# Kernel tuning notes

Hardware: AMD Instinct MI355X
Metric: run time of the kernel (lower is better)

Reference implementation:

```python
import jax, jax.numpy as jnp
import numpy as np

D = 1024
H = 16
DH = D // H  # 64
SCALE = DH ** (-0.5)

def setup_inputs() -> dict:
    key = jax.random.key(0)
    k1, k2, k3, k4, k5 = jax.random.split(key, 5)
    x = jax.random.normal(k1, (4, 2048, D), dtype=jnp.float32)
    w_qkv = jax.random.normal(k2, (D, 3 * D), dtype=jnp.float32) * (D ** -0.5)
    b_qkv = jax.random.normal(k3, (3 * D,), dtype=jnp.float32) * 0.02
    w_out = jax.random.normal(k4, (D, D), dtype=jnp.float32) * (D ** -0.5)
    b_out = jax.random.normal(k5, (D,), dtype=jnp.float32) * 0.02
    return {"x": x, "w_qkv": w_qkv, "b_qkv": b_qkv, "w_out": w_out, "b_out": b_out}

def reference(x, w_qkv, b_qkv, w_out, b_out):
    B, S, C = x.shape
    qkv = x @ w_qkv + b_qkv                          # [B,S,3D]
    qkv = qkv.reshape(B, S, 3, H, DH)
    qkv = jnp.transpose(qkv, (0, 3, 2, 1, 4))        # [B,H,3,S,DH]
    q, k, v = qkv[:, :, 0], qkv[:, :, 1], qkv[:, :, 2]
    q = q * SCALE
    scores = jnp.einsum('bhqd,bhkd->bhqk', q, k)     # [B,H,S,S]
    attn = jax.nn.softmax(scores.astype(jnp.float32), axis=-1).astype(scores.dtype)
    out = jnp.einsum('bhqk,bhkd->bhqd', attn, v)     # [B,H,S,DH]
    out = jnp.transpose(out, (0, 2, 1, 3)).reshape(B, S, C)
    return out @ w_out + b_out
```

## Files before the change

kernel.cpp:

```cpp
#include <hip/hip_runtime.h>

#define D_ 1024
#define H_ 16
#define DH_ 64
#define S_ 2048
#define B_ 4
#define N_ (B_*S_)
#define M3_ 3072
#define QSC_ 0.18033688011112042f

typedef _Float16 f16;
typedef _Float16 f16x8 __attribute__((ext_vector_type(8)));
typedef _Float16 f16x4 __attribute__((ext_vector_type(4)));
typedef _Float16 f16x2 __attribute__((ext_vector_type(2)));
typedef __fp16   h16x2 __attribute__((ext_vector_type(2)));
typedef float    f32x4 __attribute__((ext_vector_type(4)));

typedef __attribute__((address_space(1))) void gvoid;
typedef __attribute__((address_space(3))) void lvoid;

__device__ __forceinline__ void gl16(const f16* g, f16* l) {
    __builtin_amdgcn_global_load_lds((gvoid*)g, (lvoid*)l, 16, 0, 0);
}

__device__ __forceinline__ f16x2 pk_cvt(float a, float b) {
#if __has_builtin(__builtin_amdgcn_cvt_pkrtz)
    h16x2 t = __builtin_amdgcn_cvt_pkrtz(a, b);
    return __builtin_bit_cast(f16x2, t);
#else
    f16x2 r; r[0] = (f16)a; r[1] = (f16)b; return r;
#endif
}

__device__ __forceinline__ float dot2acc(f16x2 a, float acc) {
#if __has_builtin(__builtin_amdgcn_fdot2)
    h16x2 one; one[0] = (__fp16)1.f; one[1] = (__fp16)1.f;
    return __builtin_amdgcn_fdot2(__builtin_bit_cast(h16x2, a), one, acc, false);
#else
    return acc + (float)a[0] + (float)a[1];
#endif
}

__global__ __launch_bounds__(256) void cvt_x_kernel(const float* __restrict__ in,
                                                    f16* __restrict__ out) {
    size_t i = ((size_t)blockIdx.x * 256 + threadIdx.x) * 4;
    float4 f = *reinterpret_cast<const float4*>(in + i);
    f16x4 o;
    o[0] = (f16)f.x; o[1] = (f16)f.y; o[2] = (f16)f.z; o[3] = (f16)f.w;
    *reinterpret_cast<f16x4*>(out + i) = o;
}

__global__ __launch_bounds__(256) void wt_cvt_kernel(const float* __restrict__ in,
                                                     f16* __restrict__ out,
                                                     int K, int Nc) {
    __shared__ float tile[32][33];
    int tx = threadIdx.x & 31, ty = threadIdx.x >> 5;
    int c = blockIdx.x * 32 + tx;
    #pragma unroll
    for (int i = 0; i < 4; i++) {
        int r = blockIdx.y * 32 + ty + i * 8;
        tile[ty + i * 8][tx] = in[(size_t)r * Nc + c];
    }
    __syncthreads();
    #pragma unroll
    for (int i = 0; i < 4; i++) {
        int r2 = blockIdx.x * 32 + ty + i * 8;
        int c2 = blockIdx.y * 32 + tx;
        out[(size_t)r2 * K + c2] = (f16)tile[tx][ty + i * 8];
    }
}

__global__ __launch_bounds__(256) void gemm_qkv_kernel(
        const f16* __restrict__ A, const f16* __restrict__ Bt,
        const float* __restrict__ bias,
        f16* __restrict__ qo, f16* __restrict__ ko, f16* __restrict__ vTo) {
    __shared__ __align__(16) f16 As[128 * 32];
    __shared__ __align__(16) f16 Bs[128 * 32];
    const int tid  = threadIdx.x;
    const int lane = tid & 63, w = tid >> 6;
    const int quad = lane >> 4, lrow = lane & 15;
    const int wm = (w & 1) * 64, wn = (w >> 1) * 64;
    const int n0 = blockIdx.x * 128, m0 = blockIdx.y * 128;

    f32x4 acc[4][4];
    #pragma unroll
    for (int i = 0; i < 4; i++)
        #pragma unroll
        for (int j = 0; j < 4; j++) acc[i][j] = {0.f, 0.f, 0.f, 0.f};

    const int ar0 = tid >> 2, ap0 = tid & 3;
    const f16* Ag0 = A  + (size_t)(n0 + ar0) * D_ + ap0 * 8;
    const f16* Ag1 = Ag0 + (size_t)64 * D_;
    const f16* Bg0 = Bt + (size_t)(m0 + ar0) * D_ + ap0 * 8;
    const f16* Bg1 = Bg0 + (size_t)64 * D_;
    f16* Asl = As + tid * 8;
    f16* Bsl = Bs + tid * 8;

    for (int kt = 0; kt < D_ / 32; kt++) {
        gl16(Ag0 + kt * 32, Asl);
        gl16(Ag1 + kt * 32, Asl + 64 * 32);
        gl16(Bg0 + kt * 32, Bsl);
        gl16(Bg1 + kt * 32, Bsl + 64 * 32);
        __syncthreads();
        f16x8 af[4], bf[4];
        #pragma unroll
        for (int i = 0; i < 4; i++)
            af[i] = *reinterpret_cast<const f16x8*>(&As[(wm + i * 16 + lrow) * 32 + quad * 8]);
        #pragma unroll
        for (int j = 0; j < 4; j++)
            bf[j] = *reinterpret_cast<const f16x8*>(&Bs[(wn + j * 16 + lrow) * 32 + quad * 8]);
        #pragma unroll
        for (int i = 0; i < 4; i++)
            #pragma unroll
            for (int j = 0; j < 4; j++)
                acc[i][j] = __builtin_amdgcn_mfma_f32_16x16x32_f16(af[i], bf[j], acc[i][j], 0, 0, 0);
        __syncthreads();
    }

    #pragma unroll
    for (int j = 0; j < 4; j++) {
        int m   = m0 + wn + j * 16 + lrow;
        int sec = m >> 10;
        int hd  = m & 1023;
        int hh  = hd >> 6, d = hd & 63;
        float bb = bias[m];
        if (sec == 2) {
            #pragma unroll
            for (int i = 0; i < 4; i++) {
                int n = n0 + wm + i * 16 + quad * 4;
                int bidx = n >> 11, s = n & 2047;
                f16x4 o;
                #pragma unroll
                for (int r = 0; r < 4; r++) o[r] = (f16)(acc[i][j][r] + bb);
                *reinterpret_cast<f16x4*>(
                    &vTo[(((size_t)(bidx * H_ + hh)) * DH_ + d) * S_ + s]) = o;
            }
        } else {
            f16* dst = (sec == 0) ? qo : ko;
            float sc = (sec == 0) ? QSC_ : 1.0f;
            #pragma unroll
            for (int i = 0; i < 4; i++) {
                #pragma unroll
                for (int r = 0; r < 4; r++) {
                    int n = n0 + wm + i * 16 + quad * 4 + r;
                    int bidx = n >> 11, s = n & 2047;
                    dst[(((size_t)(bidx * H_ + hh)) * S_ + s) * DH_ + d] =
                        (f16)((acc[i][j][r] + bb) * sc);
                }
            }
        }
    }
}

__global__ __launch_bounds__(256) void attn_kernel(
        const f16* __restrict__ q, const f16* __restrict__ k,
        const f16* __restrict__ vT, f16* __restrict__ ctx) {
    __shared__ __align__(16) f16 Ks[128 * 72];
    __shared__ __align__(16) f16 Vs[64 * 136];
    const int tid  = threadIdx.x;
    const int lane = tid & 63, w = tid >> 6;
    const int quad = lane >> 4, lrow = lane & 15;
    const int bh = blockIdx.y;
    const int b  = bh >> 4, h = bh & 15;
    const int q0 = blockIdx.x * 256;
    const f16* qb = q  + (size_t)bh * S_ * DH_;
    const f16* kb = k  + (size_t)bh * S_ * DH_;
    const f16* vb = vT + (size_t)bh * DH_ * S_;

    f16x8 qf[4][2];
    #pragma unroll
    for (int f = 0; f < 4; f++)
        #pragma unroll
        for (int hf = 0; hf < 2; hf++)
            qf[f][hf] = *reinterpret_cast<const f16x8*>(
                qb + (size_t)(q0 + w * 64 + f * 16 + lrow) * DH_ + hf * 32 + quad * 8);

    float l_i[4] = {0.f, 0.f, 0.f, 0.f};
    f32x4 ot[4][4];
    #pragma unroll
    for (int f = 0; f < 4; f++)
        #pragma unroll
        for (int dj = 0; dj < 4; dj++) ot[f][dj] = {0.f, 0.f, 0.f, 0.f};

    int kslot[4], kpart[4], vrow[4], vpart[4];
    #pragma unroll
    for (int i = 0; i < 4; i++) {
        int ch = tid + i * 256;
        int g = ch >> 3, jj = g & 7, qd = (g >> 3) & 3;
        kslot[i] = (g & ~31) + ((jj >> 2) << 4) + (qd << 2) + (jj & 3);
        kpart[i] = ch & 7;
        vrow[i] = ch >> 4; vpart[i] = ch & 15;
    }

    f16x8 krg[4], vrg[4];
    #pragma unroll
    for (int i = 0; i < 4; i++) {
        int ch = tid + i * 256;
        krg[i] = *reinterpret_cast<const f16x8*>(kb + (size_t)(ch >> 3) * DH_ + (ch & 7) * 8);
        vrg[i] = *reinterpret_cast<const f16x8*>(vb + (size_t)vrow[i] * S_ + vpart[i] * 8);
    }

    for (int kt = 0; kt < S_ / 128; kt++) {
        #pragma unroll
        for (int i = 0; i < 4; i++) {
            *reinterpret_cast<f16x8*>(&Ks[kslot[i] * 72 + kpart[i] * 8]) = krg[i];
            *reinterpret_cast<f16x8*>(&Vs[vrow[i] * 136 + vpart[i] * 8]) = vrg[i];
        }
        __syncthreads();
        if (kt + 1 < S_ / 128) {
            const int kv1 = (kt + 1) * 128;
            #pragma unroll
            for (int i = 0; i < 4; i++) {
                int ch = tid + i * 256;
                krg[i] = *reinterpret_cast<const f16x8*>(kb + (size_t)(kv1 + (ch >> 3)) * DH_ + (ch & 7) * 8);
                vrg[i] = *reinterpret_cast<const f16x8*>(vb + (size_t)vrow[i] * S_ + kv1 + vpart[i] * 8);
            }
        }

        #pragma unroll
        for (int t = 0; t < 4; t++) {
            f16x8 p8[4];
            #pragma unroll
            for (int half = 0; half < 2; half++) {
                int mb = 2 * t + half;
                f16x8 kf0 = *reinterpret_cast<const f16x8*>(&Ks[(mb * 16 + lrow) * 72 + quad * 8]);
                f16x8 kf1 = *reinterpret_cast<const f16x8*>(&Ks[(mb * 16 + lrow) * 72 + 32 + quad * 8]);
                #pragma unroll
                for (int f = 0; f < 4; f++) {
                    f32x4 st = {0.f, 0.f, 0.f, 0.f};
                    st = __builtin_amdgcn_mfma_f32_16x16x32_f16(kf0, qf[f][0], st, 0, 0, 0);
                    st = __builtin_amdgcn_mfma_f32_16x16x32_f16(kf1, qf[f][1], st, 0, 0, 0);
                    f16x2 lo = pk_cvt(__builtin_amdgcn_exp2f(st[0]),
                                      __builtin_amdgcn_exp2f(st[1]));
                    f16x2 hi = pk_cvt(__builtin_amdgcn_exp2f(st[2]),
                                      __builtin_amdgcn_exp2f(st[3]));
                    l_i[f] = dot2acc(lo, l_i[f]);
                    l_i[f] = dot2acc(hi, l_i[f]);
                    p8[f][half * 4 + 0] = lo[0]; p8[f][half * 4 + 1] = lo[1];
                    p8[f][half * 4 + 2] = hi[0]; p8[f][half * 4 + 3] = hi[1];
                }
            }
            #pragma unroll
            for (int dj = 0; dj < 4; dj++) {
                f16x8 vf = *reinterpret_cast<const f16x8*>(
                    &Vs[(dj * 16 + lrow) * 136 + t * 32 + quad * 8]);
                #pragma unroll
                for (int f = 0; f < 4; f++)
                    ot[f][dj] = __builtin_amdgcn_mfma_f32_16x16x32_f16(vf, p8[f], ot[f][dj], 0, 0, 0);
            }
        }
        __syncthreads();
    }

    #pragma unroll
    for (int f = 0; f < 4; f++) {
        float l = l_i[f];
        l += __shfl_xor(l, 16);
        l += __shfl_xor(l, 32);
        float inv = 1.0f / l;
        int qrow = q0 + w * 64 + f * 16 + lrow;
        #pragma unroll
        for (int dj = 0; dj < 4; dj++) {
            f16x4 o;
            #pragma unroll
            for (int r = 0; r < 4; r++) o[r] = (f16)(ot[f][dj][r] * inv);
            *reinterpret_cast<f16x4*>(
                &ctx[((size_t)(b * S_ + qrow)) * D_ + h * DH_ + dj * 16 + quad * 4]) = o;
        }
    }
}

__global__ __launch_bounds__(256) void gemm_out_kernel(
        const f16* __restrict__ A, const f16* __restrict__ Bt,
        const float* __restrict__ bias, float* __restrict__ out) {
    __shared__ __align__(16) f16 As[128 * 32];
    __shared__ __align__(16) f16 Bs[128 * 32];
    const int tid  = threadIdx.x;
    const int lane = tid & 63, w = tid >> 6;
    const int quad = lane >> 4, lrow = lane & 15;
    const int wm = (w & 1) * 64, wn = (w >> 1) * 64;
    const int n0 = blockIdx.x * 128, m0 = blockIdx.y * 128;

    f32x4 acc[4][4];
    #pragma unroll
    for (int i = 0; i < 4; i++)
        #pragma unroll
        for (int j = 0; j < 4; j++) acc[i][j] = {0.f, 0.f, 0.f, 0.f};

    const int ar0 = tid >> 2, ap0 = tid & 3;
    const f16* Ag0 = A  + (size_t)(n0 + ar0) * D_ + ap0 * 8;
    const f16* Ag1 = Ag0 + (size_t)64 * D_;
    const f16* Bg0 = Bt + (size_t)(m0 + ar0) * D_ + ap0 * 8;
    const f16* Bg1 = Bg0 + (size_t)64 * D_;
    f16* Asl = As + tid * 8;
    f16* Bsl = Bs + tid * 8;

    for (int kt = 0; kt < D_ / 32; kt++) {
        gl16(Ag0 + kt * 32, Asl);
        gl16(Ag1 + kt * 32, Asl + 64 * 32);
        gl16(Bg0 + kt * 32, Bsl);
        gl16(Bg1 + kt * 32, Bsl + 64 * 32);
        __syncthreads();
        f16x8 af[4], bf[4];
        #pragma unroll
        for (int i = 0; i < 4; i++)
            af[i] = *reinterpret_cast<const f16x8*>(&As[(wm + i * 16 + lrow) * 32 + quad * 8]);
        #pragma unroll
        for (int j = 0; j < 4; j++)
            bf[j] = *reinterpret_cast<const f16x8*>(&Bs[(wn + j * 16 + lrow) * 32 + quad * 8]);
        #pragma unroll
        for (int i = 0; i < 4; i++)
            #pragma unroll
            for (int j = 0; j < 4; j++)
                acc[i][j] = __builtin_amdgcn_mfma_f32_16x16x32_f16(af[i], bf[j], acc[i][j], 0, 0, 0);
        __syncthreads();
    }

    #pragma unroll
    for (int j = 0; j < 4; j++) {
        int m = m0 + wn + j * 16 + lrow;
        float bb = bias[m];
        #pragma unroll
        for (int i = 0; i < 4; i++)
            #pragma unroll
            for (int r = 0; r < 4; r++) {
                int n = n0 + wm + i * 16 + quad * 4 + r;
                out[(size_t)n * D_ + m] = acc[i][j][r] + bb;
            }
    }
}

extern "C" void kernel_launch(void* const* d_in, const int* in_sizes, int n_in,
                              void* d_out, int out_size, void* d_ws, size_t ws_size,
                              hipStream_t stream) {
    (void)in_sizes; (void)n_in; (void)out_size; (void)ws_size;
    const float* x     = (const float*)d_in[0];
    const float* w_qkv = (const float*)d_in[1];
    const float* b_qkv = (const float*)d_in[2];
    const float* w_out = (const float*)d_in[3];
    const float* b_out = (const float*)d_in[4];
    float* out = (float*)d_out;

    char* ws = (char*)d_ws;
    const size_t MB = 1024 * 1024;
    f16* xb    = (f16*)(ws);
    f16* wqkvT = (f16*)(ws + 16 * MB);
    f16* woutT = (f16*)(ws + 22 * MB);
    f16* qs    = (f16*)(ws + 24 * MB);
    f16* kk    = (f16*)(ws + 40 * MB);
    f16* vTb   = (f16*)(ws + 72 * MB);
    f16* ctx   = xb;

    cvt_x_kernel<<<(N_ * D_) / (256 * 4), 256, 0, stream>>>(x, xb);
    wt_cvt_kernel<<<dim3(M3_ / 32, D_ / 32), 256, 0, stream>>>(w_qkv, wqkvT, D_, M3_);
    wt_cvt_kernel<<<dim3(D_ / 32, D_ / 32), 256, 0, stream>>>(w_out, woutT, D_, D_);
    gemm_qkv_kernel<<<dim3(N_ / 128, M3_ / 128), 256, 0, stream>>>(xb, wqkvT, b_qkv, qs, kk, vTb);
    attn_kernel<<<dim3(S_ / 256, B_ * H_), 256, 0, stream>>>(qs, kk, vTb, ctx);
    gemm_out_kernel<<<dim3(N_ / 128, D_ / 128), 256, 0, stream>>>(ctx, woutT, b_out, out);
}
```

Measured before the change: 274.9 us.

## Load attention K/V fragments directly from global memory, drop LDS staging

The attention kernel no longer stages K and V tiles through shared memory with barriers. Each lane now loads its MFMA fragments straight from global memory, relying on L2/L1 caching because the four waves read the same K/V data. The 1-D grid is remapped so blocks on the same head are spread across XCDs to improve L2 locality. This removes the LDS writes and syncthreads, but adds redundant global/cache traffic and exposes memory latency, since there is no software prefetch.

```diff
diff --git a/kernel.cpp b/kernel.cpp
--- a/kernel.cpp
+++ b/kernel.cpp
@@ -155,14 +155,13 @@
 __global__ __launch_bounds__(256) void attn_kernel(
         const f16* __restrict__ q, const f16* __restrict__ k,
         const f16* __restrict__ vT, f16* __restrict__ ctx) {
-    __shared__ __align__(16) f16 Ks[128 * 72];
-    __shared__ __align__(16) f16 Vs[64 * 136];
     const int tid  = threadIdx.x;
     const int lane = tid & 63, w = tid >> 6;
     const int quad = lane >> 4, lrow = lane & 15;
-    const int bh = blockIdx.y;
+    const int id = blockIdx.x;
+    const int bh = (id & 7) * 8 + (id >> 6);
     const int b  = bh >> 4, h = bh & 15;
-    const int q0 = blockIdx.x * 256;
+    const int q0 = ((id >> 3) & 7) * 256;
     const f16* qb = q  + (size_t)bh * S_ * DH_;
     const f16* kb = k  + (size_t)bh * S_ * DH_;
     const f16* vb = vT + (size_t)bh * DH_ * S_;
@@ -182,49 +181,23 @@
         #pragma unroll
         for (int dj = 0; dj < 4; dj++) ot[f][dj] = {0.f, 0.f, 0.f, 0.f};
 
-    int kslot[4], kpart[4], vrow[4], vpart[4];
-    #pragma unroll
-    for (int i = 0; i < 4; i++) {
-        int ch = tid + i * 256;
-        int g = ch >> 3, jj = g & 7, qd = (g >> 3) & 3;
-        kslot[i] = (g & ~31) + ((jj >> 2) << 4) + (qd << 2) + (jj & 3);
-        kpart[i] = ch & 7;
-        vrow[i] = ch >> 4; vpart[i] = ch & 15;
-    }
-
-    f16x8 krg[4], vrg[4];
-    #pragma unroll
-    for (int i = 0; i < 4; i++) {
-        int ch = tid + i * 256;
-        krg[i] = *reinterpret_cast<const f16x8*>(kb + (size_t)(ch >> 3) * DH_ + (ch & 7) * 8);
-        vrg[i] = *reinterpret_cast<const f16x8*>(vb + (size_t)vrow[i] * S_ + vpart[i] * 8);
-    }
+    const int krow_lane = ((lrow >> 2) << 3) + (lrow & 3);
+    const f16* kl = kb + (size_t)krow_lane * DH_ + quad * 8;
+    const f16* vl[4];
+    #pragma unroll
+    for (int dj = 0; dj < 4; dj++)
+        vl[dj] = vb + (size_t)(dj * 16 + lrow) * S_ + quad * 8;
 
     for (int kt = 0; kt < S_ / 128; kt++) {
-        #pragma unroll
-        for (int i = 0; i < 4; i++) {
-            *reinterpret_cast<f16x8*>(&Ks[kslot[i] * 72 + kpart[i] * 8]) = krg[i];
-            *reinterpret_cast<f16x8*>(&Vs[vrow[i] * 136 + vpart[i] * 8]) = vrg[i];
-        }
-        __syncthreads();
-        if (kt + 1 < S_ / 128) {
-            const int kv1 = (kt + 1) * 128;
-            #pragma unroll
-            for (int i = 0; i < 4; i++) {
-                int ch = tid + i * 256;
-                krg[i] = *reinterpret_cast<const f16x8*>(kb + (size_t)(kv1 + (ch >> 3)) * DH_ + (ch & 7) * 8);
-                vrg[i] = *reinterpret_cast<const f16x8*>(vb + (size_t)vrow[i] * S_ + kv1 + vpart[i] * 8);
-            }
-        }
-
+        const int kv0 = kt * 128;
         #pragma unroll
         for (int t = 0; t < 4; t++) {
             f16x8 p8[4];
             #pragma unroll
             for (int half = 0; half < 2; half++) {
-                int mb = 2 * t + half;
-                f16x8 kf0 = *reinterpret_cast<const f16x8*>(&Ks[(mb * 16 + lrow) * 72 + quad * 8]);
-                f16x8 kf1 = *reinterpret_cast<const f16x8*>(&Ks[(mb * 16 + lrow) * 72 + 32 + quad * 8]);
+                const f16* kr = kl + (size_t)(kv0 + t * 32 + half * 4) * DH_;
+                f16x8 kf0 = *reinterpret_cast<const f16x8*>(kr);
+                f16x8 kf1 = *reinterpret_cast<const f16x8*>(kr + 32);
                 #pragma unroll
                 for (int f = 0; f < 4; f++) {
                     f32x4 st = {0.f, 0.f, 0.f, 0.f};
@@ -242,14 +215,12 @@
             }
             #pragma unroll
             for (int dj = 0; dj < 4; dj++) {
-                f16x8 vf = *reinterpret_cast<const f16x8*>(
-                    &Vs[(dj * 16 + lrow) * 136 + t * 32 + quad * 8]);
+                f16x8 vf = *reinterpret_cast<const f16x8*>(vl[dj] + kv0 + t * 32);
                 #pragma unroll
                 for (int f = 0; f < 4; f++)
                     ot[f][dj] = __builtin_amdgcn_mfma_f32_16x16x32_f16(vf, p8[f], ot[f][dj], 0, 0, 0);
             }
         }
-        __syncthreads();
     }
 
     #pragma unroll
@@ -355,6 +326,6 @@
     wt_cvt_kernel<<<dim3(M3_ / 32, D_ / 32), 256, 0, stream>>>(w_qkv, wqkvT, D_, M3_);
     wt_cvt_kernel<<<dim3(D_ / 32, D_ / 32), 256, 0, stream>>>(w_out, woutT, D_, D_);
     gemm_qkv_kernel<<<dim3(N_ / 128, M3_ / 128), 256, 0, stream>>>(xb, wqkvT, b_qkv, qs, kk, vTb);
-    attn_kernel<<<dim3(S_ / 256, B_ * H_), 256, 0, stream>>>(qs, kk, vTb, ctx);
+    attn_kernel<<<(B_ * H_ * S_) / 256, 256, 0, stream>>>(qs, kk, vTb, ctx);
     gemm_out_kernel<<<dim3(N_ / 128, D_ / 128), 256, 0, stream>>>(ctx, woutT, b_out, out);
 }
```

Result: slower. 330.3 us (+20.2%).

## Double-buffer attention K/V tiles, compute row sums via MFMA, remap grid

Applied to the files above, without the earlier changes.

The attention kernel now keeps two LDS buffers for K and V. The next tile is written while the current one is consumed, which removes one barrier per iteration. The softmax row sum is no longer accumulated with scalar dot2 instructions; an extra MFMA against a ones vector produces it, and that also removes the final cross-lane shuffles. The grid becomes 1-D with the head index in the low bits, so blocks that run together cover different heads. The cost is double the LDS use, which may lower occupancy, plus extra MFMA work.

```diff
diff --git a/kernel.cpp b/kernel.cpp
--- a/kernel.cpp
+++ b/kernel.cpp
@@ -29,15 +29,6 @@
     return __builtin_bit_cast(f16x2, t);
 #else
     f16x2 r; r[0] = (f16)a; r[1] = (f16)b; return r;
-#endif
-}
-
-__device__ __forceinline__ float dot2acc(f16x2 a, float acc) {
-#if __has_builtin(__builtin_amdgcn_fdot2)
-    h16x2 one; one[0] = (__fp16)1.f; one[1] = (__fp16)1.f;
-    return __builtin_amdgcn_fdot2(__builtin_bit_cast(h16x2, a), one, acc, false);
-#else
-    return acc + (float)a[0] + (float)a[1];
 #endif
 }
 
@@ -155,14 +146,15 @@
 __global__ __launch_bounds__(256) void attn_kernel(
         const f16* __restrict__ q, const f16* __restrict__ k,
         const f16* __restrict__ vT, f16* __restrict__ ctx) {
-    __shared__ __align__(16) f16 Ks[128 * 72];
-    __shared__ __align__(16) f16 Vs[64 * 136];
+    __shared__ __align__(16) f16 Ks[2][128 * 72];
+    __shared__ __align__(16) f16 Vs[2][64 * 136];
     const int tid  = threadIdx.x;
     const int lane = tid & 63, w = tid >> 6;
     const int quad = lane >> 4, lrow = lane & 15;
-    const int bh = blockIdx.y;
+    const int id = blockIdx.x;
+    const int bh = id & 63;
+    const int q0 = (id >> 6) * 256;
     const int b  = bh >> 4, h = bh & 15;
-    const int q0 = blockIdx.x * 256;
     const f16* qb = q  + (size_t)bh * S_ * DH_;
     const f16* kb = k  + (size_t)bh * S_ * DH_;
     const f16* vb = vT + (size_t)bh * DH_ * S_;
@@ -175,12 +167,18 @@
             qf[f][hf] = *reinterpret_cast<const f16x8*>(
                 qb + (size_t)(q0 + w * 64 + f * 16 + lrow) * DH_ + hf * 32 + quad * 8);
 
-    float l_i[4] = {0.f, 0.f, 0.f, 0.f};
+    f16x8 ones8;
+    #pragma unroll
+    for (int i = 0; i < 8; i++) ones8[i] = (f16)1.f;
+
+    f32x4 lacc[4];
     f32x4 ot[4][4];
     #pragma unroll
-    for (int f = 0; f < 4; f++)
+    for (int f = 0; f < 4; f++) {
+        lacc[f] = {0.f, 0.f, 0.f, 0.f};
         #pragma unroll
         for (int dj = 0; dj < 4; dj++) ot[f][dj] = {0.f, 0.f, 0.f, 0.f};
+    }
 
     int kslot[4], kpart[4], vrow[4], vpart[4];
     #pragma unroll
@@ -199,23 +197,24 @@
         krg[i] = *reinterpret_cast<const f16x8*>(kb + (size_t)(ch >> 3) * DH_ + (ch & 7) * 8);
         vrg[i] = *reinterpret_cast<const f16x8*>(vb + (size_t)vrow[i] * S_ + vpart[i] * 8);
     }
-
-    for (int kt = 0; kt < S_ / 128; kt++) {
-        #pragma unroll
-        for (int i = 0; i < 4; i++) {
-            *reinterpret_cast<f16x8*>(&Ks[kslot[i] * 72 + kpart[i] * 8]) = krg[i];
-            *reinterpret_cast<f16x8*>(&Vs[vrow[i] * 136 + vpart[i] * 8]) = vrg[i];
-        }
-        __syncthreads();
-        if (kt + 1 < S_ / 128) {
-            const int kv1 = (kt + 1) * 128;
-            #pragma unroll
-            for (int i = 0; i < 4; i++) {
-                int ch = tid + i * 256;
-                krg[i] = *reinterpret_cast<const f16x8*>(kb + (size_t)(kv1 + (ch >> 3)) * DH_ + (ch & 7) * 8);
-                vrg[i] = *reinterpret_cast<const f16x8*>(vb + (size_t)vrow[i] * S_ + kv1 + vpart[i] * 8);
-            }
-        }
+    #pragma unroll
+    for (int i = 0; i < 4; i++) {
+        *reinterpret_cast<f16x8*>(&Ks[0][kslot[i] * 72 + kpart[i] * 8]) = krg[i];
+        *reinterpret_cast<f16x8*>(&Vs[0][vrow[i] * 136 + vpart[i] * 8]) = vrg[i];
+    }
+    #pragma unroll
+    for (int i = 0; i < 4; i++) {
+        int ch = tid + i * 256;
+        krg[i] = *reinterpret_cast<const f16x8*>(kb + (size_t)(128 + (ch >> 3)) * DH_ + (ch & 7) * 8);
+        vrg[i] = *reinterpret_cast<const f16x8*>(vb + (size_t)vrow[i] * S_ + 128 + vpart[i] * 8);
+    }
+    __syncthreads();
+
+    const int NT = S_ / 128;
+    for (int kt = 0; kt < NT; kt++) {
+        const int cur = kt & 1;
+        const f16* Kc = Ks[cur];
+        const f16* Vc = Vs[cur];
 
         #pragma unroll
         for (int t = 0; t < 4; t++) {
@@ -223,8 +222,8 @@
             #pragma unroll
             for (int half = 0; half < 2; half++) {
                 int mb = 2 * t + half;
-                f16x8 kf0 = *reinterpret_cast<const f16x8*>(&Ks[(mb * 16 + lrow) * 72 + quad * 8]);
-                f16x8 kf1 = *reinterpret_cast<const f16x8*>(&Ks[(mb * 16 + lrow) * 72 + 32 + quad * 8]);
+                f16x8 kf0 = *reinterpret_cast<const f16x8*>(&Kc[(mb * 16 + lrow) * 72 + quad * 8]);
+                f16x8 kf1 = *reinterpret_cast<const f16x8*>(&Kc[(mb * 16 + lrow) * 72 + 32 + quad * 8]);
                 #pragma unroll
                 for (int f = 0; f < 4; f++) {
                     f32x4 st = {0.f, 0.f, 0.f, 0.f};
@@ -234,8 +233,6 @@
                                       __builtin_amdgcn_exp2f(st[1]));
                     f16x2 hi = pk_cvt(__builtin_amdgcn_exp2f(st[2]),
                                       __builtin_amdgcn_exp2f(st[3]));
-                    l_i[f] = dot2acc(lo, l_i[f]);
-                    l_i[f] = dot2acc(hi, l_i[f]);
                     p8[f][half * 4 + 0] = lo[0]; p8[f][half * 4 + 1] = lo[1];
                     p8[f][half * 4 + 2] = hi[0]; p8[f][half * 4 + 3] = hi[1];
                 }
@@ -243,21 +240,39 @@
             #pragma unroll
             for (int dj = 0; dj < 4; dj++) {
                 f16x8 vf = *reinterpret_cast<const f16x8*>(
-                    &Vs[(dj * 16 + lrow) * 136 + t * 32 + quad * 8]);
+                    &Vc[(dj * 16 + lrow) * 136 + t * 32 + quad * 8]);
                 #pragma unroll
                 for (int f = 0; f < 4; f++)
                     ot[f][dj] = __builtin_amdgcn_mfma_f32_16x16x32_f16(vf, p8[f], ot[f][dj], 0, 0, 0);
             }
+            #pragma unroll
+            for (int f = 0; f < 4; f++)
+                lacc[f] = __builtin_amdgcn_mfma_f32_16x16x32_f16(ones8, p8[f], lacc[f], 0, 0, 0);
         }
-        __syncthreads();
+
+        if (kt + 1 < NT) {
+            const int nxt = cur ^ 1;
+            #pragma unroll
+            for (int i = 0; i < 4; i++) {
+                *reinterpret_cast<f16x8*>(&Ks[nxt][kslot[i] * 72 + kpart[i] * 8]) = krg[i];
+                *reinterpret_cast<f16x8*>(&Vs[nxt][vrow[i] * 136 + vpart[i] * 8]) = vrg[i];
+            }
+            if (kt + 2 < NT) {
+                const int kv2 = (kt + 2) * 128;
+                #pragma unroll
+                for (int i = 0; i < 4; i++) {
+                    int ch = tid + i * 256;
+                    krg[i] = *reinterpret_cast<const f16x8*>(kb + (size_t)(kv2 + (ch >> 3)) * DH_ + (ch & 7) * 8);
+                    vrg[i] = *reinterpret_cast<const f16x8*>(vb + (size_t)vrow[i] * S_ + kv2 + vpart[i] * 8);
+                }
+            }
+            __syncthreads();
+        }
     }
 
     #pragma unroll
     for (int f = 0; f < 4; f++) {
-        float l = l_i[f];
-        l += __shfl_xor(l, 16);
-        l += __shfl_xor(l, 32);
-        float inv = 1.0f / l;
+        float inv = 1.0f / lacc[f][0];
         int qrow = q0 + w * 64 + f * 16 + lrow;
         #pragma unroll
         for (int dj = 0; dj < 4; dj++) {
@@ -355,6 +370,6 @@
     wt_cvt_kernel<<<dim3(M3_ / 32, D_ / 32), 256, 0, stream>>>(w_qkv, wqkvT, D_, M3_);
     wt_cvt_kernel<<<dim3(D_ / 32, D_ / 32), 256, 0, stream>>>(w_out, woutT, D_, D_);
     gemm_qkv_kernel<<<dim3(N_ / 128, M3_ / 128), 256, 0, stream>>>(xb, wqkvT, b_qkv, qs, kk, vTb);
-    attn_kernel<<<dim3(S_ / 256, B_ * H_), 256, 0, stream>>>(qs, kk, vTb, ctx);
+    attn_kernel<<<(B_ * H_) * (S_ / 256), 256, 0, stream>>>(qs, kk, vTb, ctx);
     gemm_out_kernel<<<dim3(N_ / 128, D_ / 128), 256, 0, stream>>>(ctx, woutT, b_out, out);
 }
```

After: 270.8 us. Within noise of the previous version (-1.5%).
